# Performance work log

Hardware: AMD Instinct MI355X
Metric: run time of the kernel (lower is better)

Reference implementation:

```python
import jax, jax.numpy as jnp
import numpy as np

VOCAB, EMB, LAT, MAXLEN, BATCH = 2048, 256, 64, 32, 64
SIZE_LAT = 3.0  # size_lat_dim: initial upper bound of every latent dimension


def setup_inputs() -> dict:
    key = jax.random.key(0)
    k0, k1, k2, k3 = jax.random.split(key, 4)
    tokens = jax.random.randint(k0, (BATCH, MAXLEN), 1, VOCAB, dtype=jnp.int32)  # avoid PAD=0
    emb = jax.random.normal(k1, (VOCAB, EMB), jnp.float32) * 0.02
    Wx = jax.random.normal(k2, (EMB, 4 * VOCAB), jnp.float32) * (1.0 / np.sqrt(EMB))
    Wh = jax.random.normal(k3, (VOCAB, 4 * VOCAB), jnp.float32) * (1.0 / np.sqrt(VOCAB))
    b = jnp.zeros((4 * VOCAB,), jnp.float32)
    return {"tokens": tokens, "emb": emb, "Wx": Wx, "Wh": Wh, "b": b}


def _lstm_step(x, h, c, Wx, Wh, b):
    # Keras LSTM gate order: i, f, g(candidate), o
    z = x @ Wx + h @ Wh + b
    i, f, g, o = jnp.split(z, 4, axis=-1)
    c = jax.nn.sigmoid(f) * c + jax.nn.sigmoid(i) * jnp.tanh(g)
    h = jax.nn.sigmoid(o) * jnp.tanh(c)
    return h, c


def reference(tokens, emb, Wx, Wh, b):
    B = tokens.shape[0]
    low0 = jnp.zeros((B, LAT), jnp.float32)
    upp0 = jnp.full((B, LAT), SIZE_LAT, jnp.float32)
    h0 = jnp.zeros((B, VOCAB), jnp.float32)  # empty (all-PAD) prefix -> zero LSTM output -> uniform softmax
    c0 = jnp.zeros((B, VOCAB), jnp.float32)
    dims = jnp.arange(LAT)

    def step(carry, tok):
        low, upp, h, c, d = carry
        # LM distribution over next token given prefix consumed so far
        probs = jax.nn.softmax(h, axis=-1)                      # [B, V]
        cum = jnp.cumsum(probs, axis=-1)
        c_upp = jnp.take_along_axis(cum, tok[:, None], axis=-1)[:, 0]
        c_low = c_upp - jnp.take_along_axis(probs, tok[:, None], axis=-1)[:, 0]
        # arithmetic-coding bound update on current latent dimension d only
        mask = dims == d                                         # [LAT]
        rng = jnp.sum(jnp.where(mask, upp - low, 0.0), axis=-1)  # [B] range at dim d
        base = jnp.sum(jnp.where(mask, low, 0.0), axis=-1)       # [B] low at dim d
        low = jnp.where(mask[None, :], (base + rng * c_low)[:, None], low)
        upp = jnp.where(mask[None, :], (base + rng * c_upp)[:, None], upp)
        z = 0.5 * (low + upp)                                    # mean of stacked bounds
        # advance embedded LM by one token (equivalent to re-running it on the prefix)
        h, c = _lstm_step(emb[tok], h, c, Wx, Wh, b)
        d = (d + 1) % LAT
        return (low, upp, h, c, d), z

    _, zs = jax.lax.scan(step, (low0, upp0, h0, c0, jnp.int32(0)), tokens.T)
    return jnp.transpose(zs, (1, 0, 2))  # [B, MAXLEN, LAT]
```

## Files before the change

kernel.cpp:

```cpp
#include <hip/hip_runtime.h>
#include <hip/hip_bf16.h>

#define VOCAB 2048
#define EMBD  256
#define LATD  64
#define TLEN  32
#define BATCH 64
#define NBLK  256
#define NCG   128

typedef __attribute__((ext_vector_type(8))) short bf16x8;
typedef __attribute__((ext_vector_type(4))) float f32x4;

__global__ void k_init(ushort* __restrict__ h0, unsigned* __restrict__ arrv) {
  int i = blockIdx.x * 256 + threadIdx.x;
  h0[i] = 0;
  if (i < 384) arrv[i] = 0;
}

__global__ void k_transpose(const float* __restrict__ src,
                            __hip_bfloat16* __restrict__ dst, int K) {
  __shared__ __hip_bfloat16 tile[64][72];
  int k0 = (blockIdx.x >> 7) * 64;
  int n0 = (blockIdx.x & 127) * 64;
  int tid = threadIdx.x;
  {
    int kl = tid >> 2;
    int nq = (tid & 3) << 4;
    const float* s = src + (size_t)(k0 + kl) * 8192 + n0 + nq;
#pragma unroll
    for (int i = 0; i < 4; ++i) {
      float4 v = *reinterpret_cast<const float4*>(s + i * 4);
      tile[nq + i * 4 + 0][kl] = __float2bfloat16(v.x);
      tile[nq + i * 4 + 1][kl] = __float2bfloat16(v.y);
      tile[nq + i * 4 + 2][kl] = __float2bfloat16(v.z);
      tile[nq + i * 4 + 3][kl] = __float2bfloat16(v.w);
    }
  }
  __syncthreads();
  {
    int nl = tid >> 2;
    int kq = (tid & 3) << 4;
    uint4* d = reinterpret_cast<uint4*>(dst + (size_t)(n0 + nl) * K + k0 + kq);
    const uint4* s = reinterpret_cast<const uint4*>(&tile[nl][kq]);
    d[0] = s[0];
    d[1] = s[1];
  }
}

__global__ void k_gather(const int* __restrict__ tokens,
                         const float* __restrict__ emb,
                         __hip_bfloat16* __restrict__ xb) {
  int tid = threadIdx.x;
  int row = blockIdx.x * 4 + (tid >> 6);
  int lane = tid & 63;
  int t = row >> 6, b = row & 63;
  int tok = tokens[b * TLEN + t];
  float4 v = *reinterpret_cast<const float4*>(emb + (size_t)tok * EMBD + lane * 4);
  __hip_bfloat16* d = xb + (size_t)row * EMBD + lane * 4;
  d[0] = __float2bfloat16(v.x);
  d[1] = __float2bfloat16(v.y);
  d[2] = __float2bfloat16(v.z);
  d[3] = __float2bfloat16(v.w);
}

__device__ __forceinline__ void store_agent_u32(unsigned* p, unsigned v) {
  __hip_atomic_store(p, v, __ATOMIC_RELAXED, __HIP_MEMORY_SCOPE_AGENT);
}
__device__ __forceinline__ unsigned load_agent_u32(const unsigned* p) {
  return __hip_atomic_load(p, __ATOMIC_RELAXED, __HIP_MEMORY_SCOPE_AGENT);
}
__device__ __forceinline__ unsigned long long load_agent_u64(const void* p) {
  return __hip_atomic_load((const unsigned long long*)p, __ATOMIC_RELAXED,
                           __HIP_MEMORY_SCOPE_AGENT);
}
__device__ __forceinline__ void store_agent_f32(float* p, float v) {
  __hip_atomic_store(p, v, __ATOMIC_RELAXED, __HIP_MEMORY_SCOPE_AGENT);
}
__device__ __forceinline__ float2 load_agent_f32x2(const float* p) {
  unsigned long long u = load_agent_u64(p);
  float2 f;
  __builtin_memcpy(&f, &u, 8);
  return f;
}
__device__ __forceinline__ unsigned short bf16_bits(float x) {
  __hip_bfloat16 h = __float2bfloat16(x);
  unsigned short u;
  __builtin_memcpy(&u, &h, 2);
  return u;
}

__device__ __forceinline__ void grid_barrier(unsigned* arrv, unsigned* rel,
                                             int t, int j, int tid, int lane) {
  __syncthreads();
  const unsigned want = (unsigned)(t + 1);
  if (j == 0) {
    if (tid < 64) {
      if (lane == 0) store_agent_u32(arrv, want);
      for (;;) {
        unsigned long long a = load_agent_u64(arrv + 2 * lane);
        unsigned long long b = load_agent_u64(arrv + 128 + 2 * lane);
        bool ok = ((unsigned)a >= want) && ((unsigned)(a >> 32) >= want) &&
                  ((unsigned)b >= want) && ((unsigned)(b >> 32) >= want);
        if (__all(ok)) break;
      }
      if (lane < 8) store_agent_u32(rel + (lane << 4), want);
    }
  } else {
    if (tid == 0) {
      store_agent_u32(arrv + j, want);
      while (load_agent_u32(rel + ((j & 7) << 4)) < want)
        __builtin_amdgcn_s_sleep(1);
    }
  }
  __syncthreads();
}

__global__ __launch_bounds__(512, 1) void k_persist(
    const int* __restrict__ tokens,
    const __hip_bfloat16* __restrict__ WhT,
    const __hip_bfloat16* __restrict__ WxT,
    const __hip_bfloat16* __restrict__ xb,
    const float* __restrict__ bias,
    __hip_bfloat16* __restrict__ hring,
    float* __restrict__ stats,
    float* __restrict__ out,
    unsigned* __restrict__ arrv,
    unsigned* __restrict__ rel) {
  const int tid = threadIdx.x;
  const int lane = tid & 63;
  const int wid = tid >> 6;
  const int j = blockIdx.x;
  const int cg = (j & 7) | ((j >> 4) << 3);
  const int rg = (j >> 3) & 1;
  const int r0 = rg << 5;

  __shared__ float racc[8][2][4][4][64];
  __shared__ float spart[TLEN][3];
  __shared__ float sval[TLEN];

  const int rr = lane & 15;
  const int kg = lane >> 4;

  const __hip_bfloat16* bBase[4];
#pragma unroll
  for (int gt = 0; gt < 4; ++gt)
    bBase[gt] = WhT + (size_t)((gt << 11) + (cg << 4) + rr) * VOCAB + wid * 256 + kg * 8;
  const __hip_bfloat16* bxBase[4];
#pragma unroll
  for (int gt = 0; gt < 4; ++gt)
    bxBase[gt] = WxT + (size_t)((gt << 11) + (cg << 4) + rr) * EMBD + wid * 32 + kg * 8;

  const int m_e = wid >> 2;
  const int r_e = wid & 3;
  const int rowg = r0 + m_e * 16 + kg * 4 + r_e;
  const int v = (cg << 4) + rr;
  float bias_r[4];
#pragma unroll
  for (int gt = 0; gt < 4; ++gt) bias_r[gt] = bias[gt * 2048 + v];
  float c_reg = 0.f;

  for (int t = 0; t < TLEN; ++t) {
    const int par = t & 1;
    const __hip_bfloat16* hcur = hring + (size_t)t * (BATCH * VOCAB);
    __hip_bfloat16* hnext = (__hip_bfloat16*)hring + (size_t)(t + 1) * (BATCH * VOCAB);
    const int tnext = (t + 1 < TLEN) ? t + 1 : TLEN - 1;
    const int tok = tokens[rowg * TLEN + tnext];

    float2 sv;
    const bool do_stat = (t > 0) && (j < BATCH) && (wid < 3);
    if (do_stat)
      sv = load_agent_f32x2(stats + par * 3 * BATCH * NCG +
                            (wid * BATCH + j) * NCG + lane * 2);

    f32x4 acc[2][4];
#pragma unroll
    for (int mf = 0; mf < 2; ++mf)
#pragma unroll
      for (int gt = 0; gt < 4; ++gt) acc[mf][gt] = (f32x4){0.f, 0.f, 0.f, 0.f};

    const __hip_bfloat16* aBase = hcur + (size_t)(r0 + rr) * VOCAB + wid * 256 + kg * 8;
    const __hip_bfloat16* xBase = xb + (size_t)t * BATCH * EMBD +
                                  (size_t)(r0 + rr) * EMBD + wid * 32 + kg * 8;
    bf16x8 Ar[4][2];
    bf16x8 Br[4][4];
    auto issue = [&](int it) {
      int slot = it & 3;
      if (it < 8) {
        Ar[slot][0] = *(const bf16x8*)(aBase + it * 32);
        Ar[slot][1] = *(const bf16x8*)(aBase + 16 * VOCAB + it * 32);
#pragma unroll
        for (int gt = 0; gt < 4; ++gt)
          Br[slot][gt] = *(const bf16x8*)(bBase[gt] + it * 32);
      } else {
        Ar[slot][0] = *(const bf16x8*)(xBase);
        Ar[slot][1] = *(const bf16x8*)(xBase + 16 * EMBD);
#pragma unroll
        for (int gt = 0; gt < 4; ++gt)
          Br[slot][gt] = *(const bf16x8*)(bxBase[gt]);
      }
    };

#pragma unroll
    for (int it = 0; it < 4; ++it) issue(it);
#pragma unroll
    for (int it = 0; it < 9; ++it) {
      const int sl = it & 3;
#pragma unroll
      for (int gt = 0; gt < 4; ++gt) {
        acc[0][gt] = __builtin_amdgcn_mfma_f32_16x16x32_bf16(Ar[sl][0], Br[sl][gt], acc[0][gt], 0, 0, 0);
        acc[1][gt] = __builtin_amdgcn_mfma_f32_16x16x32_bf16(Ar[sl][1], Br[sl][gt], acc[1][gt], 0, 0, 0);
      }
      if (it + 4 < 9) issue(it + 4);
    }

#pragma unroll
    for (int mf = 0; mf < 2; ++mf)
#pragma unroll
      for (int gt = 0; gt < 4; ++gt)
#pragma unroll
        for (int r = 0; r < 4; ++r) racc[wid][mf][gt][r][lane] = acc[mf][gt][r];
    __syncthreads();

    if (do_stat) {
      float a = sv.x + sv.y;
#pragma unroll
      for (int mm = 1; mm <= 32; mm <<= 1) a += __shfl_xor(a, mm);
      if (lane == 0) spart[t][wid] = a;
    }

    float z[4];
#pragma unroll
    for (int gt = 0; gt < 4; ++gt) {
      float s = bias_r[gt];
#pragma unroll
      for (int w = 0; w < 8; ++w) s += racc[w][m_e][gt][r_e][lane];
      z[gt] = s;
    }
    float gi = 1.f / (1.f + __expf(-z[0]));
    float gf = 1.f / (1.f + __expf(-z[1]));
    float go = 1.f / (1.f + __expf(-z[3]));
    float cnew = gf * c_reg + gi * tanhf(z[2]);
    float hn = go * tanhf(cnew);
    c_reg = cnew;

    {
      unsigned b0 = bf16_bits(hn);
      unsigned q0 = (unsigned)__shfl_xor((int)b0, 1);
      if (!(rr & 1))
        store_agent_u32((unsigned*)(hnext + rowg * VOCAB + v), b0 | (q0 << 16));
    }

    float e = __expf(hn);
    float sl = (v < tok) ? e : 0.f;
    float st = (v == tok) ? e : 0.f;
#pragma unroll
    for (int mm = 1; mm <= 8; mm <<= 1) {
      e += __shfl_xor(e, mm);
      sl += __shfl_xor(sl, mm);
      st += __shfl_xor(st, mm);
    }
    if (rr == 0) {
      float* stn = stats + (par ^ 1) * 3 * BATCH * NCG;
      store_agent_f32(&stn[(0 * BATCH + rowg) * NCG + cg], e);
      store_agent_f32(&stn[(1 * BATCH + rowg) * NCG + cg], sl);
      store_agent_f32(&stn[(2 * BATCH + rowg) * NCG + cg], st);
    }

    if (t < TLEN - 1) grid_barrier(arrv, rel, t, j, tid, lane);
  }

  if (j < BATCH) {
    __syncthreads();
    if (tid < TLEN) {
      float val;
      if (tid == 0) {
        int tk = tokens[j * TLEN];
        val = 1.5f * (2.f * tk + 1.f) * (1.f / 2048.f);
      } else {
        float S  = spart[tid][0];
        float SL = spart[tid][1];
        float ST = spart[tid][2];
        val = 1.5f * (2.f * SL + ST) / S;
      }
      sval[tid] = val;
    }
    __syncthreads();
    for (int idx = tid; idx < TLEN * LATD; idx += 512) {
      int tp = idx >> 6, d = idx & 63;
      out[j * TLEN * LATD + idx] = (d < TLEN && d <= tp) ? sval[d] : 1.5f;
    }
  }
}

extern "C" void kernel_launch(void* const* d_in, const int* in_sizes, int n_in,
                              void* d_out, int out_size, void* d_ws, size_t ws_size,
                              hipStream_t stream) {
  (void)in_sizes; (void)n_in; (void)out_size; (void)ws_size;
  const int* tokens = (const int*)d_in[0];
  const float* emb  = (const float*)d_in[1];
  const float* Wx   = (const float*)d_in[2];
  const float* Wh   = (const float*)d_in[3];
  const float* bias = (const float*)d_in[4];
  float* out = (float*)d_out;
  char* ws = (char*)d_ws;

  __hip_bfloat16* WhT = (__hip_bfloat16*)(ws);
  __hip_bfloat16* WxT = (__hip_bfloat16*)(ws + 33554432);
  __hip_bfloat16* xb  = (__hip_bfloat16*)(ws + 37748736);
  __hip_bfloat16* hr  = (__hip_bfloat16*)(ws + 38797312);
  float* stats        = (float*)(ws + 47448064);
  unsigned* arrv      = (unsigned*)(ws + 47644672);
  unsigned* rel       = (unsigned*)(ws + 47645696);

  k_init<<<512, 256, 0, stream>>>((ushort*)hr, arrv);
  k_transpose<<<4096, 256, 0, stream>>>(Wh, WhT, 2048);
  k_transpose<<<512, 256, 0, stream>>>(Wx, WxT, 256);
  k_gather<<<512, 256, 0, stream>>>(tokens, emb, xb);
  k_persist<<<NBLK, 512, 0, stream>>>(tokens, WhT, WxT, xb, bias, hr, stats, out, arrv, rel);
}
```

Measured before the change: 270.2 us.

## Split grid barrier into independent per-row-group halves and defer stats reduction

```diff
diff --git a/kernel.cpp b/kernel.cpp
--- a/kernel.cpp
+++ b/kernel.cpp
@@ -12,10 +12,12 @@
 typedef __attribute__((ext_vector_type(8))) short bf16x8;
 typedef __attribute__((ext_vector_type(4))) float f32x4;
 
-__global__ void k_init(ushort* __restrict__ h0, unsigned* __restrict__ arrv) {
+#define BAR_WORDS 896
+
+__global__ void k_init(ushort* __restrict__ h0, unsigned* __restrict__ bar) {
   int i = blockIdx.x * 256 + threadIdx.x;
   h0[i] = 0;
-  if (i < 384) arrv[i] = 0;
+  if (i < BAR_WORDS) bar[i] = 0;
 }
 
 __global__ void k_transpose(const float* __restrict__ src,
@@ -77,12 +79,6 @@
 __device__ __forceinline__ void store_agent_f32(float* p, float v) {
   __hip_atomic_store(p, v, __ATOMIC_RELAXED, __HIP_MEMORY_SCOPE_AGENT);
 }
-__device__ __forceinline__ float2 load_agent_f32x2(const float* p) {
-  unsigned long long u = load_agent_u64(p);
-  float2 f;
-  __builtin_memcpy(&f, &u, 8);
-  return f;
-}
 __device__ __forceinline__ unsigned short bf16_bits(float x) {
   __hip_bfloat16 h = __float2bfloat16(x);
   unsigned short u;
@@ -90,26 +86,26 @@
   return u;
 }
 
-__device__ __forceinline__ void grid_barrier(unsigned* arrv, unsigned* rel,
-                                             int t, int j, int tid, int lane) {
+__device__ __forceinline__ void half_barrier(unsigned* bar, int t, int cg,
+                                             int rg, int xg, int tid, int lane) {
   __syncthreads();
   const unsigned want = (unsigned)(t + 1);
-  if (j == 0) {
+  unsigned* hArr = bar + rg * 128;
+  unsigned* hRel = bar + 256;
+  if (cg == 0) {
     if (tid < 64) {
-      if (lane == 0) store_agent_u32(arrv, want);
+      if (lane == 0) store_agent_u32(hArr, want);
       for (;;) {
-        unsigned long long a = load_agent_u64(arrv + 2 * lane);
-        unsigned long long b = load_agent_u64(arrv + 128 + 2 * lane);
-        bool ok = ((unsigned)a >= want) && ((unsigned)(a >> 32) >= want) &&
-                  ((unsigned)b >= want) && ((unsigned)(b >> 32) >= want);
+        unsigned long long a = load_agent_u64(hArr + 2 * lane);
+        bool ok = ((unsigned)a >= want) && ((unsigned)(a >> 32) >= want);
         if (__all(ok)) break;
       }
-      if (lane < 8) store_agent_u32(rel + (lane << 4), want);
+      if (lane < 8) store_agent_u32(hRel + ((rg * 8 + lane) << 4), want);
     }
   } else {
     if (tid == 0) {
-      store_agent_u32(arrv + j, want);
-      while (load_agent_u32(rel + ((j & 7) << 4)) < want)
+      store_agent_u32(hArr + cg, want);
+      while (load_agent_u32(hRel + ((rg * 8 + xg) << 4)) < want)
         __builtin_amdgcn_s_sleep(1);
     }
   }
@@ -125,18 +121,17 @@
     __hip_bfloat16* __restrict__ hring,
     float* __restrict__ stats,
     float* __restrict__ out,
-    unsigned* __restrict__ arrv,
-    unsigned* __restrict__ rel) {
+    unsigned* __restrict__ bar) {
   const int tid = threadIdx.x;
   const int lane = tid & 63;
   const int wid = tid >> 6;
   const int j = blockIdx.x;
   const int cg = (j & 7) | ((j >> 4) << 3);
   const int rg = (j >> 3) & 1;
+  const int xg = j & 7;
   const int r0 = rg << 5;
 
   __shared__ float racc[8][2][4][4][64];
-  __shared__ float spart[TLEN][3];
   __shared__ float sval[TLEN];
 
   const int rr = lane & 15;
@@ -161,17 +156,9 @@
   float c_reg = 0.f;
 
   for (int t = 0; t < TLEN; ++t) {
-    const int par = t & 1;
     const __hip_bfloat16* hcur = hring + (size_t)t * (BATCH * VOCAB);
     __hip_bfloat16* hnext = (__hip_bfloat16*)hring + (size_t)(t + 1) * (BATCH * VOCAB);
-    const int tnext = (t + 1 < TLEN) ? t + 1 : TLEN - 1;
-    const int tok = tokens[rowg * TLEN + tnext];
-
-    float2 sv;
-    const bool do_stat = (t > 0) && (j < BATCH) && (wid < 3);
-    if (do_stat)
-      sv = load_agent_f32x2(stats + par * 3 * BATCH * NCG +
-                            (wid * BATCH + j) * NCG + lane * 2);
+    const int tok = (t < TLEN - 1) ? tokens[rowg * TLEN + t + 1] : 0;
 
     f32x4 acc[2][4];
 #pragma unroll
@@ -182,10 +169,10 @@
     const __hip_bfloat16* aBase = hcur + (size_t)(r0 + rr) * VOCAB + wid * 256 + kg * 8;
     const __hip_bfloat16* xBase = xb + (size_t)t * BATCH * EMBD +
                                   (size_t)(r0 + rr) * EMBD + wid * 32 + kg * 8;
-    bf16x8 Ar[4][2];
-    bf16x8 Br[4][4];
+    bf16x8 Ar[5][2];
+    bf16x8 Br[5][4];
     auto issue = [&](int it) {
-      int slot = it & 3;
+      int slot = it % 5;
       if (it < 8) {
         Ar[slot][0] = *(const bf16x8*)(aBase + it * 32);
         Ar[slot][1] = *(const bf16x8*)(aBase + 16 * VOCAB + it * 32);
@@ -202,16 +189,16 @@
     };
 
 #pragma unroll
-    for (int it = 0; it < 4; ++it) issue(it);
+    for (int it = 0; it < 5; ++it) issue(it);
 #pragma unroll
     for (int it = 0; it < 9; ++it) {
-      const int sl = it & 3;
+      const int sl = it % 5;
 #pragma unroll
       for (int gt = 0; gt < 4; ++gt) {
         acc[0][gt] = __builtin_amdgcn_mfma_f32_16x16x32_bf16(Ar[sl][0], Br[sl][gt], acc[0][gt], 0, 0, 0);
         acc[1][gt] = __builtin_amdgcn_mfma_f32_16x16x32_bf16(Ar[sl][1], Br[sl][gt], acc[1][gt], 0, 0, 0);
       }
-      if (it + 4 < 9) issue(it + 4);
+      if (it + 5 < 9) issue(it + 5);
     }
 
 #pragma unroll
@@ -221,13 +208,6 @@
 #pragma unroll
         for (int r = 0; r < 4; ++r) racc[wid][mf][gt][r][lane] = acc[mf][gt][r];
     __syncthreads();
-
-    if (do_stat) {
-      float a = sv.x + sv.y;
-#pragma unroll
-      for (int mm = 1; mm <= 32; mm <<= 1) a += __shfl_xor(a, mm);
-      if (lane == 0) spart[t][wid] = a;
-    }
 
     float z[4];
 #pragma unroll
@@ -244,46 +224,80 @@
     float hn = go * tanhf(cnew);
     c_reg = cnew;
 
-    {
+    if (t < TLEN - 1) {
       unsigned b0 = bf16_bits(hn);
       unsigned q0 = (unsigned)__shfl_xor((int)b0, 1);
       if (!(rr & 1))
         store_agent_u32((unsigned*)(hnext + rowg * VOCAB + v), b0 | (q0 << 16));
-    }
-
-    float e = __expf(hn);
-    float sl = (v < tok) ? e : 0.f;
-    float st = (v == tok) ? e : 0.f;
-#pragma unroll
-    for (int mm = 1; mm <= 8; mm <<= 1) {
-      e += __shfl_xor(e, mm);
-      sl += __shfl_xor(sl, mm);
-      st += __shfl_xor(st, mm);
-    }
-    if (rr == 0) {
-      float* stn = stats + (par ^ 1) * 3 * BATCH * NCG;
-      store_agent_f32(&stn[(0 * BATCH + rowg) * NCG + cg], e);
-      store_agent_f32(&stn[(1 * BATCH + rowg) * NCG + cg], sl);
-      store_agent_f32(&stn[(2 * BATCH + rowg) * NCG + cg], st);
-    }
-
-    if (t < TLEN - 1) grid_barrier(arrv, rel, t, j, tid, lane);
+
+      float e = __expf(hn);
+      float sl = (v < tok) ? e : 0.f;
+      float st = (v == tok) ? e : 0.f;
+#pragma unroll
+      for (int mm = 1; mm <= 8; mm <<= 1) {
+        e += __shfl_xor(e, mm);
+        sl += __shfl_xor(sl, mm);
+        st += __shfl_xor(st, mm);
+      }
+      if (rr == 0) {
+        float* stn = stats + (size_t)t * 3 * BATCH * NCG;
+        store_agent_f32(&stn[(0 * BATCH + rowg) * NCG + cg], e);
+        store_agent_f32(&stn[(1 * BATCH + rowg) * NCG + cg], sl);
+        store_agent_f32(&stn[(2 * BATCH + rowg) * NCG + cg], st);
+      }
+
+      half_barrier(bar, t, cg, rg, xg, tid, lane);
+    }
+  }
+
+  {
+    __syncthreads();
+    unsigned* fArr = bar + 512;
+    unsigned* fRel = bar + 768;
+    if (j == 0) {
+      if (tid < 64) {
+        if (lane == 0) store_agent_u32(fArr, 1u);
+        for (;;) {
+          unsigned long long a = load_agent_u64(fArr + 2 * lane);
+          unsigned long long b = load_agent_u64(fArr + 128 + 2 * lane);
+          bool ok = ((unsigned)a >= 1u) && ((unsigned)(a >> 32) >= 1u) &&
+                    ((unsigned)b >= 1u) && ((unsigned)(b >> 32) >= 1u);
+          if (__all(ok)) break;
+        }
+        if (lane < 8) store_agent_u32(fRel + (lane << 4), 1u);
+      }
+    } else {
+      if (tid == 0) {
+        store_agent_u32(fArr + j, 1u);
+        if (j < BATCH)
+          while (load_agent_u32(fRel + ((j & 7) << 4)) < 1u)
+            __builtin_amdgcn_s_sleep(1);
+      }
+    }
+    __syncthreads();
   }
 
   if (j < BATCH) {
-    __syncthreads();
-    if (tid < TLEN) {
+    for (int tt = wid; tt < TLEN; tt += 8) {
       float val;
-      if (tid == 0) {
+      if (tt == 0) {
         int tk = tokens[j * TLEN];
         val = 1.5f * (2.f * tk + 1.f) * (1.f / 2048.f);
       } else {
-        float S  = spart[tid][0];
-        float SL = spart[tid][1];
-        float ST = spart[tid][2];
-        val = 1.5f * (2.f * SL + ST) / S;
-      }
-      sval[tid] = val;
+        const float* st = stats + (size_t)(tt - 1) * 3 * BATCH * NCG;
+        float2 u0 = *reinterpret_cast<const float2*>(st + (0 * BATCH + j) * NCG + lane * 2);
+        float2 u1 = *reinterpret_cast<const float2*>(st + (1 * BATCH + j) * NCG + lane * 2);
+        float2 u2 = *reinterpret_cast<const float2*>(st + (2 * BATCH + j) * NCG + lane * 2);
+        float a0 = u0.x + u0.y, a1 = u1.x + u1.y, a2 = u2.x + u2.y;
+#pragma unroll
+        for (int mm = 1; mm <= 32; mm <<= 1) {
+          a0 += __shfl_xor(a0, mm);
+          a1 += __shfl_xor(a1, mm);
+          a2 += __shfl_xor(a2, mm);
+        }
+        val = 1.5f * (2.f * a1 + a2) / a0;
+      }
+      if (lane == 0) sval[tt] = val;
     }
     __syncthreads();
     for (int idx = tid; idx < TLEN * LATD; idx += 512) {
@@ -310,12 +324,11 @@
   __hip_bfloat16* xb  = (__hip_bfloat16*)(ws + 37748736);
   __hip_bfloat16* hr  = (__hip_bfloat16*)(ws + 38797312);
   float* stats        = (float*)(ws + 47448064);
-  unsigned* arrv      = (unsigned*)(ws + 47644672);
-  unsigned* rel       = (unsigned*)(ws + 47645696);
-
-  k_init<<<512, 256, 0, stream>>>((ushort*)hr, arrv);
+  unsigned* bar       = (unsigned*)(ws + 50495488);
+
+  k_init<<<512, 256, 0, stream>>>((ushort*)hr, bar);
   k_transpose<<<4096, 256, 0, stream>>>(Wh, WhT, 2048);
   k_transpose<<<512, 256, 0, stream>>>(Wx, WxT, 256);
   k_gather<<<512, 256, 0, stream>>>(tokens, emb, xb);
-  k_persist<<<NBLK, 512, 0, stream>>>(tokens, WhT, WxT, xb, bias, hr, stats, out, arrv, rel);
-}
+  k_persist<<<NBLK, 512, 0, stream>>>(tokens, WhT, WxT, xb, bias, hr, stats, out, bar);
+}
```

New measurement: 272.0 us. Within noise of the previous version (+0.6%).

## Switch LSTM GEMM to FP8 with register-resident weights and fused K layout

Applied to the files above, without the earlier changes.

```diff
diff --git a/kernel.cpp b/kernel.cpp
--- a/kernel.cpp
+++ b/kernel.cpp
@@ -3,24 +3,29 @@
 
 #define VOCAB 2048
 #define EMBD  256
+#define KTOT  2304
 #define LATD  64
 #define TLEN  32
 #define BATCH 64
 #define NBLK  256
 #define NCG   128
-
-typedef __attribute__((ext_vector_type(8))) short bf16x8;
+#define AROW  2304
+#define ASLOT (BATCH * AROW)
+
 typedef __attribute__((ext_vector_type(4))) float f32x4;
 
-__global__ void k_init(ushort* __restrict__ h0, unsigned* __restrict__ arrv) {
+__global__ void k_init(unsigned char* __restrict__ a8, unsigned* __restrict__ bar) {
   int i = blockIdx.x * 256 + threadIdx.x;
-  h0[i] = 0;
-  if (i < 384) arrv[i] = 0;
-}
-
-__global__ void k_transpose(const float* __restrict__ src,
-                            __hip_bfloat16* __restrict__ dst, int K) {
-  __shared__ __hip_bfloat16 tile[64][72];
+  if (i < 32768) {
+    int row = i >> 9;
+    *(unsigned*)(a8 + (size_t)row * AROW + ((i & 511) << 2)) = 0u;
+  }
+  if (i < 384) bar[i] = 0;
+}
+
+__global__ void k_conv(const float* __restrict__ src,
+                       unsigned char* __restrict__ dst, int koff) {
+  __shared__ unsigned char tile[64][80];
   int k0 = (blockIdx.x >> 7) * 64;
   int n0 = (blockIdx.x & 127) * 64;
   int tid = threadIdx.x;
@@ -31,37 +36,36 @@
 #pragma unroll
     for (int i = 0; i < 4; ++i) {
       float4 v = *reinterpret_cast<const float4*>(s + i * 4);
-      tile[nq + i * 4 + 0][kl] = __float2bfloat16(v.x);
-      tile[nq + i * 4 + 1][kl] = __float2bfloat16(v.y);
-      tile[nq + i * 4 + 2][kl] = __float2bfloat16(v.z);
-      tile[nq + i * 4 + 3][kl] = __float2bfloat16(v.w);
+      unsigned pa = (unsigned)__builtin_amdgcn_cvt_pk_fp8_f32(v.x * 32.f, v.y * 32.f, 0, false);
+      unsigned pb = (unsigned)__builtin_amdgcn_cvt_pk_fp8_f32(v.z * 32.f, v.w * 32.f, 0, false);
+      tile[nq + i * 4 + 0][kl] = (unsigned char)(pa & 0xFF);
+      tile[nq + i * 4 + 1][kl] = (unsigned char)((pa >> 8) & 0xFF);
+      tile[nq + i * 4 + 2][kl] = (unsigned char)(pb & 0xFF);
+      tile[nq + i * 4 + 3][kl] = (unsigned char)((pb >> 8) & 0xFF);
     }
   }
   __syncthreads();
   {
     int nl = tid >> 2;
     int kq = (tid & 3) << 4;
-    uint4* d = reinterpret_cast<uint4*>(dst + (size_t)(n0 + nl) * K + k0 + kq);
-    const uint4* s = reinterpret_cast<const uint4*>(&tile[nl][kq]);
-    d[0] = s[0];
-    d[1] = s[1];
+    *(uint4*)(dst + (size_t)(n0 + nl) * AROW + koff + k0 + kq) =
+        *(const uint4*)&tile[nl][kq];
   }
 }
 
 __global__ void k_gather(const int* __restrict__ tokens,
                          const float* __restrict__ emb,
-                         __hip_bfloat16* __restrict__ xb) {
+                         unsigned char* __restrict__ a8) {
   int tid = threadIdx.x;
   int row = blockIdx.x * 4 + (tid >> 6);
   int lane = tid & 63;
   int t = row >> 6, b = row & 63;
   int tok = tokens[b * TLEN + t];
   float4 v = *reinterpret_cast<const float4*>(emb + (size_t)tok * EMBD + lane * 4);
-  __hip_bfloat16* d = xb + (size_t)row * EMBD + lane * 4;
-  d[0] = __float2bfloat16(v.x);
-  d[1] = __float2bfloat16(v.y);
-  d[2] = __float2bfloat16(v.z);
-  d[3] = __float2bfloat16(v.w);
+  unsigned pa = (unsigned)__builtin_amdgcn_cvt_pk_fp8_f32(v.x * 256.f, v.y * 256.f, 0, false);
+  unsigned pb = (unsigned)__builtin_amdgcn_cvt_pk_fp8_f32(v.z * 256.f, v.w * 256.f, 0, false);
+  *(unsigned*)(a8 + (size_t)t * ASLOT + (size_t)b * AROW + 2048 + lane * 4) =
+      (pa & 0xFFFFu) | (pb << 16);
 }
 
 __device__ __forceinline__ void store_agent_u32(unsigned* p, unsigned v) {
@@ -82,12 +86,6 @@
   float2 f;
   __builtin_memcpy(&f, &u, 8);
   return f;
-}
-__device__ __forceinline__ unsigned short bf16_bits(float x) {
-  __hip_bfloat16 h = __float2bfloat16(x);
-  unsigned short u;
-  __builtin_memcpy(&u, &h, 2);
-  return u;
 }
 
 __device__ __forceinline__ void grid_barrier(unsigned* arrv, unsigned* rel,
@@ -118,11 +116,9 @@
 
 __global__ __launch_bounds__(512, 1) void k_persist(
     const int* __restrict__ tokens,
-    const __hip_bfloat16* __restrict__ WhT,
-    const __hip_bfloat16* __restrict__ WxT,
-    const __hip_bfloat16* __restrict__ xb,
+    const unsigned char* __restrict__ B8,
+    unsigned char* __restrict__ a8,
     const float* __restrict__ bias,
-    __hip_bfloat16* __restrict__ hring,
     float* __restrict__ stats,
     float* __restrict__ out,
     unsigned* __restrict__ arrv,
@@ -142,14 +138,18 @@
   const int rr = lane & 15;
   const int kg = lane >> 4;
 
-  const __hip_bfloat16* bBase[4];
-#pragma unroll
-  for (int gt = 0; gt < 4; ++gt)
-    bBase[gt] = WhT + (size_t)((gt << 11) + (cg << 4) + rr) * VOCAB + wid * 256 + kg * 8;
-  const __hip_bfloat16* bxBase[4];
-#pragma unroll
-  for (int gt = 0; gt < 4; ++gt)
-    bxBase[gt] = WxT + (size_t)((gt << 11) + (cg << 4) + rr) * EMBD + wid * 32 + kg * 8;
+  long Bf[9][4];
+  {
+    const unsigned char* b8B[4];
+#pragma unroll
+    for (int gt = 0; gt < 4; ++gt)
+      b8B[gt] = B8 + (size_t)((gt << 11) + (cg << 4) + rr) * AROW + wid * 288 + kg * 8;
+#pragma unroll
+    for (int it = 0; it < 9; ++it)
+#pragma unroll
+      for (int gt = 0; gt < 4; ++gt)
+        Bf[it][gt] = *(const long*)(b8B[gt] + it * 32);
+  }
 
   const int m_e = wid >> 2;
   const int r_e = wid & 3;
@@ -162,8 +162,8 @@
 
   for (int t = 0; t < TLEN; ++t) {
     const int par = t & 1;
-    const __hip_bfloat16* hcur = hring + (size_t)t * (BATCH * VOCAB);
-    __hip_bfloat16* hnext = (__hip_bfloat16*)hring + (size_t)(t + 1) * (BATCH * VOCAB);
+    const unsigned char* a8cur = a8 + (size_t)t * ASLOT;
+    unsigned char* a8next = a8 + (size_t)(t + 1) * ASLOT;
     const int tnext = (t + 1 < TLEN) ? t + 1 : TLEN - 1;
     const int tok = tokens[rowg * TLEN + tnext];
 
@@ -179,26 +179,12 @@
 #pragma unroll
       for (int gt = 0; gt < 4; ++gt) acc[mf][gt] = (f32x4){0.f, 0.f, 0.f, 0.f};
 
-    const __hip_bfloat16* aBase = hcur + (size_t)(r0 + rr) * VOCAB + wid * 256 + kg * 8;
-    const __hip_bfloat16* xBase = xb + (size_t)t * BATCH * EMBD +
-                                  (size_t)(r0 + rr) * EMBD + wid * 32 + kg * 8;
-    bf16x8 Ar[4][2];
-    bf16x8 Br[4][4];
+    const unsigned char* aB = a8cur + (size_t)(r0 + rr) * AROW + wid * 288 + kg * 8;
+    long Ar[4][2];
     auto issue = [&](int it) {
       int slot = it & 3;
-      if (it < 8) {
-        Ar[slot][0] = *(const bf16x8*)(aBase + it * 32);
-        Ar[slot][1] = *(const bf16x8*)(aBase + 16 * VOCAB + it * 32);
-#pragma unroll
-        for (int gt = 0; gt < 4; ++gt)
-          Br[slot][gt] = *(const bf16x8*)(bBase[gt] + it * 32);
-      } else {
-        Ar[slot][0] = *(const bf16x8*)(xBase);
-        Ar[slot][1] = *(const bf16x8*)(xBase + 16 * EMBD);
-#pragma unroll
-        for (int gt = 0; gt < 4; ++gt)
-          Br[slot][gt] = *(const bf16x8*)(bxBase[gt]);
-      }
+      Ar[slot][0] = *(const long*)(aB + it * 32);
+      Ar[slot][1] = *(const long*)(aB + 16 * AROW + it * 32);
     };
 
 #pragma unroll
@@ -208,8 +194,8 @@
       const int sl = it & 3;
 #pragma unroll
       for (int gt = 0; gt < 4; ++gt) {
-        acc[0][gt] = __builtin_amdgcn_mfma_f32_16x16x32_bf16(Ar[sl][0], Br[sl][gt], acc[0][gt], 0, 0, 0);
-        acc[1][gt] = __builtin_amdgcn_mfma_f32_16x16x32_bf16(Ar[sl][1], Br[sl][gt], acc[1][gt], 0, 0, 0);
+        acc[0][gt] = __builtin_amdgcn_mfma_f32_16x16x32_fp8_fp8(Ar[sl][0], Bf[it][gt], acc[0][gt], 0, 0, 0);
+        acc[1][gt] = __builtin_amdgcn_mfma_f32_16x16x32_fp8_fp8(Ar[sl][1], Bf[it][gt], acc[1][gt], 0, 0, 0);
       }
       if (it + 4 < 9) issue(it + 4);
     }
@@ -232,10 +218,10 @@
     float z[4];
 #pragma unroll
     for (int gt = 0; gt < 4; ++gt) {
-      float s = bias_r[gt];
+      float s = 0.f;
 #pragma unroll
       for (int w = 0; w < 8; ++w) s += racc[w][m_e][gt][r_e][lane];
-      z[gt] = s;
+      z[gt] = s * (1.f / 8192.f) + bias_r[gt];
     }
     float gi = 1.f / (1.f + __expf(-z[0]));
     float gf = 1.f / (1.f + __expf(-z[1]));
@@ -245,10 +231,15 @@
     c_reg = cnew;
 
     {
-      unsigned b0 = bf16_bits(hn);
-      unsigned q0 = (unsigned)__shfl_xor((int)b0, 1);
-      if (!(rr & 1))
-        store_agent_u32((unsigned*)(hnext + rowg * VOCAB + v), b0 | (q0 << 16));
+      float hs = hn * 256.f;
+      float hb = __shfl_xor(hs, 1);
+      float lo = (rr & 1) ? hb : hs;
+      float hi = (rr & 1) ? hs : hb;
+      unsigned pk = (unsigned)__builtin_amdgcn_cvt_pk_fp8_f32(lo, hi, 0, false) & 0xFFFFu;
+      unsigned pk2 = (unsigned)__shfl_xor((int)pk, 2);
+      unsigned word = pk | (pk2 << 16);
+      if ((rr & 3) == 0)
+        store_agent_u32((unsigned*)(a8next + (size_t)rowg * AROW + v), word);
     }
 
     float e = __expf(hn);
@@ -305,17 +296,15 @@
   float* out = (float*)d_out;
   char* ws = (char*)d_ws;
 
-  __hip_bfloat16* WhT = (__hip_bfloat16*)(ws);
-  __hip_bfloat16* WxT = (__hip_bfloat16*)(ws + 33554432);
-  __hip_bfloat16* xb  = (__hip_bfloat16*)(ws + 37748736);
-  __hip_bfloat16* hr  = (__hip_bfloat16*)(ws + 38797312);
-  float* stats        = (float*)(ws + 47448064);
-  unsigned* arrv      = (unsigned*)(ws + 47644672);
-  unsigned* rel       = (unsigned*)(ws + 47645696);
-
-  k_init<<<512, 256, 0, stream>>>((ushort*)hr, arrv);
-  k_transpose<<<4096, 256, 0, stream>>>(Wh, WhT, 2048);
-  k_transpose<<<512, 256, 0, stream>>>(Wx, WxT, 256);
-  k_gather<<<512, 256, 0, stream>>>(tokens, emb, xb);
-  k_persist<<<NBLK, 512, 0, stream>>>(tokens, WhT, WxT, xb, bias, hr, stats, out, arrv, rel);
-}
+  unsigned char* B8 = (unsigned char*)(ws);
+  unsigned char* a8 = (unsigned char*)(ws + 18874368);
+  float* stats      = (float*)(ws + 23740416);
+  unsigned* arrv    = (unsigned*)(ws + 23937024);
+  unsigned* rel     = (unsigned*)(ws + 23938048);
+
+  k_init<<<512, 256, 0, stream>>>(a8, arrv);
+  k_conv<<<4096, 256, 0, stream>>>(Wh, B8, 0);
+  k_conv<<<512, 256, 0, stream>>>(Wx, B8, 2048);
+  k_gather<<<512, 256, 0, stream>>>(tokens, emb, a8);
+  k_persist<<<NBLK, 512, 0, stream>>>(tokens, B8, a8, bias, stats, out, arrv, rel);
+}
```

Result: faster. 258.6 us (-4.3%).
